# Kernel tuning notes

Measured on AMD Instinct MI355X. Metric: run time of the kernel, lower is better.

The kernel has to match this reference:

```python
import jax, jax.numpy as jnp
import numpy as np

N_NODES = 100000


def _segment_softmax(logits, seg, num_segments):
    # numerically stable softmax of per-edge logits grouped by destination node
    m = jax.ops.segment_max(logits, seg, num_segments=num_segments)
    e = jnp.exp(logits - m[seg])
    s = jax.ops.segment_sum(e, seg, num_segments=num_segments)
    return e / s[seg]


def _cgat(x, W, b, src, dst, edge_attr, num_nodes):
    # get_edge_att: softmax of edge_attr over edges sharing a destination node
    att = _segment_softmax(edge_attr, dst, num_nodes)
    xw = x @ W.T                                  # [N, out]
    msg = att[:, None] * xw[src]                  # gather + scale  [E, out]
    aggr = jax.ops.segment_sum(msg, dst, num_segments=num_nodes)  # scatter-add
    out = aggr + xw + b                           # update(aggr, x) then + bias
    return jax.nn.sigmoid(out)


def setup_inputs() -> dict:
    key = jax.random.key(0)
    k1, k2, k3, k4, k5, k6 = jax.random.split(key, 6)
    in_c, hid_c, out_c = 128, 64, 64
    n_edges = 1600000
    x = jax.random.normal(k1, (N_NODES, in_c), dtype=jnp.float32)
    edge_index = jax.random.randint(k2, (2, n_edges), 0, N_NODES, dtype=jnp.int64)
    edge_attr = jax.random.uniform(k3, (n_edges,), dtype=jnp.float32)
    W1 = jax.random.normal(k4, (hid_c, in_c), dtype=jnp.float32) / np.sqrt(in_c)
    b1 = jnp.zeros((hid_c,), dtype=jnp.float32)
    W2 = jax.random.normal(k5, (out_c, hid_c), dtype=jnp.float32) / np.sqrt(hid_c)
    b2 = jnp.zeros((out_c,), dtype=jnp.float32)
    return {"x": x, "edge_index": edge_index, "edge_attr": edge_attr,
            "W1": W1, "b1": b1, "W2": W2, "b2": b2}


def reference(x, edge_index, edge_attr, W1, b1, W2, b2):
    src, dst = edge_index[0], edge_index[1]
    h1 = _cgat(x, W1, b1, src, dst, edge_attr, N_NODES)
    h2 = _cgat(h1, W2, b2, src, dst, edge_attr, N_NODES)
    return h2
```

## Files before the change

### kernel.cpp

```cpp
#include <hip/hip_runtime.h>
#include <hip/hip_bf16.h>

#define N_NODES 100000
#define N_EDGES 1600000
#define IN_C 128
#define C 64
#define NBKT 196
#define CAP 9216
#define BCHK 6400
#define NBB (N_EDGES / BCHK)
#define GB1 (N_NODES / 32)

typedef float vfloat2 __attribute__((ext_vector_type(2)));

__device__ __forceinline__ float bfu2f(unsigned short u) {
    return __uint_as_float(((unsigned int)u) << 16);
}
__device__ __forceinline__ unsigned short f2bfu(float f) {
    __hip_bfloat16 h = __float2bfloat16(f);
    unsigned short u; __builtin_memcpy(&u, &h, 2); return u;
}
__device__ __forceinline__ float blo(unsigned int v) { return __uint_as_float(v << 16); }
__device__ __forceinline__ float bhi(unsigned int v) { return __uint_as_float(v & 0xFFFF0000u); }
__device__ __forceinline__ float dec_w(unsigned int p) {
    return __uint_as_float(((p & 0x7FFFu) + 0x1FC000u) << 9);
}
__device__ __forceinline__ float load_f(const void* p, int i, int f32) {
    return f32 ? ((const float*)p)[i] : bfu2f(((const unsigned short*)p)[i]);
}
__device__ __forceinline__ int load_idx(const void* ei, size_t i, int i64) {
    return i64 ? (int)((const long long*)ei)[i] : ((const int*)ei)[i];
}

__global__ __launch_bounds__(256) void k_detect(
    const uint4* __restrict__ x4, const int* __restrict__ ei32,
    int* __restrict__ flags)
{
    __shared__ int cff, cnz;
    int t = threadIdx.x;
    if (t == 0) { cff = 0; cnz = 0; }
    __syncthreads();
    int lff = 0;
    #pragma unroll
    for (int j = 0; j < 16; ++j) {
        uint4 w = x4[t + j * 256];
        unsigned int a[4] = {w.x, w.y, w.z, w.w};
        #pragma unroll
        for (int q = 0; q < 4; ++q) {
            if ((a[q] & 0x00007F80u) == 0x00007F80u) lff++;
            if ((a[q] & 0x7F800000u) == 0x7F800000u) lff++;
        }
    }
    int lnz = 0;
    for (int i = t; i < 2048; i += 256)
        if (ei32[2 * i + 1] != 0) lnz++;
    if (lff) atomicAdd(&cff, lff);
    if (lnz) atomicAdd(&cnz, lnz);
    __syncthreads();
    if (t == 0) {
        flags[0] = (cff > 0) ? 1 : 0;
        flags[1] = (cnz == 0) ? 1 : 0;
    }
}

#define W1_STRIDE (IN_C + 4)
__global__ __launch_bounds__(256) void k_build_gemm1(
    const void* __restrict__ ea, const void* __restrict__ ei,
    const int* __restrict__ flags, int* __restrict__ gcnt,
    int2* __restrict__ bkt,
    const void* __restrict__ x, const void* __restrict__ W,
    unsigned short* __restrict__ xw)
{
    __shared__ __align__(16) char smem[56576];
    int t = threadIdx.x;
    if (blockIdx.x < NBB) {
        int2* stage = (int2*)smem;
        int*  h     = (int*)(smem + 51200);
        int*  ex    = (int*)(smem + 52224);
        int*  gb    = (int*)(smem + 53248);
        int*  ps    = (int*)(smem + 54272);
        int*  rk    = (int*)(smem + 55296);
        h[t] = 0; rk[t] = 0;
        __syncthreads();
        int i64 = flags[1], f32 = flags[0];
        int base = blockIdx.x * BCHK;
        for (int i = 0; i < 25; ++i) {
            int e = base + i * 256 + t;
            int d = load_idx(ei, (size_t)N_EDGES + e, i64);
            atomicAdd(&h[d >> 9], 1);
        }
        __syncthreads();
        int hv = h[t];
        ps[t] = hv;
        for (int off = 1; off < 256; off <<= 1) {
            __syncthreads();
            int val = (t >= off) ? ps[t - off] : 0;
            __syncthreads();
            ps[t] += val;
        }
        __syncthreads();
        ex[t] = ps[t] - hv;
        if (t < NBKT) gb[t] = atomicAdd(&gcnt[t], hv);
        __syncthreads();
        for (int i = 0; i < 25; ++i) {
            int e = base + i * 256 + t;
            int d = load_idx(ei, (size_t)N_EDGES + e, i64);
            int s = load_idx(ei, (size_t)e, i64);
            float w = expf(load_f(ea, e, f32));
            unsigned int wb = __float_as_uint(w);
            int wq = (int)((wb + 0x100u) >> 9) - 0x1FC000;
            wq = wq < 0 ? 0 : (wq > 0x7FFF ? 0x7FFF : wq);
            int bk2 = d >> 9;
            int r = atomicAdd(&rk[bk2], 1);
            stage[ex[bk2] + r] =
                make_int2((int)(((unsigned int)s << 15) | (unsigned int)wq), d);
        }
        __syncthreads();
        for (int i = 0; i < 25; ++i) {
            int idx = i * 256 + t;
            int2 r = stage[idx];
            int bk2 = ((unsigned int)r.y) >> 9;
            int lr = idx - ex[bk2];
            int gi = gb[bk2] + lr;
            if (gi < CAP)
                bkt[(size_t)bk2 * CAP + gi] = r;
        }
    } else {
        int bx = blockIdx.x - NBB;
        float* Wls = (float*)smem;
        float* xs  = (float*)(smem + 33792);
        int f32 = flags[0];
        size_t xbase = (size_t)bx * 32 * IN_C;
        if (f32) {
            const float* xp = (const float*)x + xbase;
            #pragma unroll
            for (int j = 0; j < 16; ++j) { int i = t + j * 256; xs[i] = xp[i]; }
            const float* wp = (const float*)W;
            #pragma unroll
            for (int j = 0; j < 32; ++j) {
                int i = t + j * 256;
                Wls[(i >> 7) * W1_STRIDE + (i & 127)] = wp[i];
            }
        } else {
            const unsigned int* xp = (const unsigned int*)((const unsigned short*)x + xbase);
            #pragma unroll
            for (int j = 0; j < 8; ++j) {
                int i = t + j * 256;
                unsigned int v = xp[i];
                xs[2 * i]     = blo(v);
                xs[2 * i + 1] = bhi(v);
            }
            const unsigned short* wp = (const unsigned short*)W;
            #pragma unroll
            for (int j = 0; j < 32; ++j) {
                int i = t + j * 256;
                Wls[(i >> 7) * W1_STRIDE + (i & 127)] = bfu2f(wp[i]);
            }
        }
        __syncthreads();
        int col = t & 63, wv = t >> 6;
        const float* wr = Wls + col * W1_STRIDE;
        const float* xr = xs + wv * 8 * IN_C;
        float acc[8];
        #pragma unroll
        for (int n = 0; n < 8; ++n) acc[n] = 0.f;
        #pragma unroll
        for (int kk = 0; kk < IN_C / 4; ++kk) {
            float4 w4 = *(const float4*)(wr + kk * 4);
            #pragma unroll
            for (int n = 0; n < 8; ++n) {
                float4 x4 = *(const float4*)(xr + n * IN_C + kk * 4);
                acc[n] += x4.x * w4.x + x4.y * w4.y + x4.z * w4.z + x4.w * w4.w;
            }
        }
        size_t obase = (size_t)bx * 32 * C + wv * 8 * C + col;
        #pragma unroll
        for (int n = 0; n < 8; ++n) xw[obase + n * C] = f2bfu(acc[n]);
    }
}

__global__ __launch_bounds__(256) void k_fine(
    const int2* __restrict__ bkt, const int* __restrict__ gcnt,
    int* __restrict__ row_ptr, unsigned int* __restrict__ srt)
{
    __shared__ int h[512], ex[512], ps[256];
    __shared__ int sh_cb;
    int t = threadIdx.x, b = blockIdx.x;
    int v = (t < NBKT) ? gcnt[t] : 0;
    ps[t] = v;
    for (int off = 1; off < 256; off <<= 1) {
        __syncthreads();
        int val = (t >= off) ? ps[t - off] : 0;
        __syncthreads();
        ps[t] += val;
    }
    __syncthreads();
    if (t == b) sh_cb = ps[t] - v;
    if (b == 0 && t == 0) row_ptr[N_NODES] = N_EDGES;
    h[t] = 0; h[t + 256] = 0;
    __syncthreads();
    int nrec = gcnt[b];
    nrec = nrec < CAP ? nrec : CAP;
    int cb = sh_cb;
    const int2* bp = bkt + (size_t)b * CAP;
    for (int i = t; i < nrec; i += 256)
        atomicAdd(&h[bp[i].y & 511], 1);
    __syncthreads();
    int s0 = h[2 * t], s1 = h[2 * t + 1];
    ps[t] = s0 + s1;
    for (int off = 1; off < 256; off <<= 1) {
        __syncthreads();
        int val = (t >= off) ? ps[t - off] : 0;
        __syncthreads();
        ps[t] += val;
    }
    __syncthreads();
    int pe = t ? ps[t - 1] : 0;
    ex[2 * t] = pe; ex[2 * t + 1] = pe + s0;
    __syncthreads();
    int d0 = b * 512 + t;
    if (d0 < N_NODES) row_ptr[d0] = cb + ex[t];
    int d1 = d0 + 256;
    if (d1 < N_NODES) row_ptr[d1] = cb + ex[t + 256];
    h[t] = 0; h[t + 256] = 0;
    __syncthreads();
    for (int i = t; i < nrec; i += 256) {
        int2 r = bp[i];
        int dl = r.y & 511;
        int rk = atomicAdd(&h[dl], 1);
        srt[cb + ex[dl] + rk] = (unsigned int)r.x;
    }
}

#define W2_STRIDE (C + 4)
__global__ __launch_bounds__(256) void k_gemm2(
    const unsigned int* __restrict__ h, const void* __restrict__ W,
    const int* __restrict__ flags, unsigned short* __restrict__ xw)
{
    __shared__ float Wls[C * W2_STRIDE];
    __shared__ float xs[32 * C];
    int t = threadIdx.x;
    size_t dwbase = (size_t)blockIdx.x * 32 * 32;
    #pragma unroll
    for (int j = 0; j < 4; ++j) {
        int i = t + j * 256;
        unsigned int v = h[dwbase + i];
        xs[2 * i]     = blo(v);
        xs[2 * i + 1] = bhi(v);
    }
    if (flags[0]) {
        const float* wp = (const float*)W;
        #pragma unroll
        for (int j = 0; j < 16; ++j) {
            int i = t + j * 256;
            Wls[(i >> 6) * W2_STRIDE + (i & 63)] = wp[i];
        }
    } else {
        const unsigned short* wp = (const unsigned short*)W;
        #pragma unroll
        for (int j = 0; j < 16; ++j) {
            int i = t + j * 256;
            Wls[(i >> 6) * W2_STRIDE + (i & 63)] = bfu2f(wp[i]);
        }
    }
    __syncthreads();
    int col = t & 63, wv = t >> 6;
    const float* wr = Wls + col * W2_STRIDE;
    const float* xr = xs + wv * 8 * C;
    float acc[8];
    #pragma unroll
    for (int n = 0; n < 8; ++n) acc[n] = 0.f;
    #pragma unroll
    for (int kk = 0; kk < C / 4; ++kk) {
        float4 w4 = *(const float4*)(wr + kk * 4);
        #pragma unroll
        for (int n = 0; n < 8; ++n) {
            float4 x4 = *(const float4*)(xr + n * C + kk * 4);
            acc[n] += x4.x * w4.x + x4.y * w4.y + x4.z * w4.z + x4.w * w4.w;
        }
    }
    size_t obase = (size_t)blockIdx.x * 32 * C + wv * 8 * C + col;
    #pragma unroll
    for (int n = 0; n < 8; ++n) xw[obase + n * C] = f2bfu(acc[n]);
}

__global__ __launch_bounds__(256) void k_msg_csr(
    const unsigned int* __restrict__ xw, const unsigned int* __restrict__ srt,
    const int* __restrict__ row_ptr, const void* __restrict__ b,
    const int* __restrict__ flags, void* __restrict__ outp, int out_is_final)
{
    int d = blockIdx.x * 4 + (threadIdx.x >> 6);
    int lane = threadIdx.x & 63;
    int half = lane >> 5, li = lane & 31;
    int beg = row_ptr[d], end = row_ptr[d + 1];
    float accx = 0.f, accy = 0.f, asum = 0.f;
    int j = beg;
    for (; j + 8 <= end; j += 8) {
        int jb = j + 4 * half;
        unsigned int p0 = __builtin_nontemporal_load(srt + jb);
        unsigned int p1 = __builtin_nontemporal_load(srt + jb + 1);
        unsigned int p2 = __builtin_nontemporal_load(srt + jb + 2);
        unsigned int p3 = __builtin_nontemporal_load(srt + jb + 3);
        unsigned int v0 = xw[(size_t)(p0 >> 15) * 32 + li];
        unsigned int v1 = xw[(size_t)(p1 >> 15) * 32 + li];
        unsigned int v2 = xw[(size_t)(p2 >> 15) * 32 + li];
        unsigned int v3 = xw[(size_t)(p3 >> 15) * 32 + li];
        float w0 = dec_w(p0), w1 = dec_w(p1), w2 = dec_w(p2), w3 = dec_w(p3);
        accx += w0 * blo(v0) + w1 * blo(v1) + w2 * blo(v2) + w3 * blo(v3);
        accy += w0 * bhi(v0) + w1 * bhi(v1) + w2 * bhi(v2) + w3 * bhi(v3);
        asum += (w0 + w1) + (w2 + w3);
    }
    if (j + 4 <= end) {
        int jb = j + 2 * half;
        unsigned int p0 = __builtin_nontemporal_load(srt + jb);
        unsigned int p1 = __builtin_nontemporal_load(srt + jb + 1);
        unsigned int v0 = xw[(size_t)(p0 >> 15) * 32 + li];
        unsigned int v1 = xw[(size_t)(p1 >> 15) * 32 + li];
        float w0 = dec_w(p0), w1 = dec_w(p1);
        accx += w0 * blo(v0) + w1 * blo(v1);
        accy += w0 * bhi(v0) + w1 * bhi(v1);
        asum += w0 + w1;
        j += 4;
    }
    if (j + 2 <= end) {
        unsigned int p0 = __builtin_nontemporal_load(srt + j + half);
        unsigned int v0 = xw[(size_t)(p0 >> 15) * 32 + li];
        float w0 = dec_w(p0);
        accx += w0 * blo(v0);
        accy += w0 * bhi(v0);
        asum += w0;
        j += 2;
    }
    if (j < end && half == 0) {
        unsigned int p0 = __builtin_nontemporal_load(srt + j);
        unsigned int v0 = xw[(size_t)(p0 >> 15) * 32 + li];
        float w0 = dec_w(p0);
        accx += w0 * blo(v0);
        accy += w0 * bhi(v0);
        asum += w0;
    }
    accx += __shfl_xor(accx, 32);
    accy += __shfl_xor(accy, 32);
    asum += __shfl_xor(asum, 32);
    float inv = (end > beg) ? 1.f / asum : 0.f;
    unsigned int sv = xw[(size_t)d * 32 + li];
    int f32 = flags[0];
    float b0 = load_f(b, 2 * li, f32), b1 = load_f(b, 2 * li + 1, f32);
    float v0 = accx * inv + blo(sv) + b0;
    float v1 = accy * inv + bhi(sv) + b1;
    float r0 = 1.f / (1.f + expf(-v0));
    float r1 = 1.f / (1.f + expf(-v1));
    if (half == 0) {
        if (out_is_final && f32) {
            vfloat2 rv; rv.x = r0; rv.y = r1;
            __builtin_nontemporal_store(rv, (vfloat2*)outp + (size_t)d * 32 + li);
        } else {
            unsigned int packed = (unsigned int)f2bfu(r0) | ((unsigned int)f2bfu(r1) << 16);
            __builtin_nontemporal_store(packed, (unsigned int*)outp + (size_t)d * 32 + li);
        }
    }
}

extern "C" void kernel_launch(void* const* d_in, const int* in_sizes, int n_in,
                              void* d_out, int out_size, void* d_ws, size_t ws_size,
                              hipStream_t stream) {
    const void* x  = d_in[0];
    const void* ei = d_in[1];
    const void* ea = d_in[2];
    const void* W1 = d_in[3];
    const void* b1 = d_in[4];
    const void* W2 = d_in[5];
    const void* b2 = d_in[6];

    char* base = (char*)d_ws;
    int*            flags   = (int*)base;
    int*            gcnt    = (int*)(base + 256);
    int*            row_ptr = (int*)(base + 4096);
    unsigned int*   srt     = (unsigned int*)(base + 405504);
    int2*           bkt     = (int2*)(base + 6805504);
    unsigned short* h1      = (unsigned short*)(base + 6805504);
    unsigned short* xw      = (unsigned short*)(base + 21256192);

    k_detect<<<1, 256, 0, stream>>>((const uint4*)x, (const int*)ei, flags);
    hipMemsetAsync(gcnt, 0, 1024, stream);

    k_build_gemm1<<<NBB + GB1, 256, 0, stream>>>(ea, ei, flags, gcnt, bkt,
                                                 x, W1, xw);
    k_fine<<<NBKT, 256, 0, stream>>>(bkt, gcnt, row_ptr, srt);

    k_msg_csr<<<N_NODES / 4, 256, 0, stream>>>((const unsigned int*)xw, srt, row_ptr, b1, flags, h1, 0);

    k_gemm2<<<N_NODES / 32, 256, 0, stream>>>((const unsigned int*)h1, W2, flags, xw);
    k_msg_csr<<<N_NODES / 4, 256, 0, stream>>>((const unsigned int*)xw, srt, row_ptr, b2, flags, d_out, 1);
}
```

Baseline: 324.7 us.

## Shrink build/gemm1 shared memory for occupancy and fold gcnt zeroing into detect

Reduces the bucketing chunk from 6400 to 4000 edges per block and splits the GEMM1 weight staging into two 32-column halves, cutting static shared memory from about 56KB to about 37KB so more blocks can be resident per CU. The zeroing of the global bucket counters moves from a separate memset into the detect kernel, removing one launch. The GEMM now loads W twice with extra barriers and each thread computes fewer outputs, which lowers reuse per block.

```diff
diff --git a/kernel.cpp b/kernel.cpp
--- a/kernel.cpp
+++ b/kernel.cpp
@@ -7,7 +7,7 @@
 #define C 64
 #define NBKT 196
 #define CAP 9216
-#define BCHK 6400
+#define BCHK 4000
 #define NBB (N_EDGES / BCHK)
 #define GB1 (N_NODES / 32)
 
@@ -34,10 +34,11 @@
 
 __global__ __launch_bounds__(256) void k_detect(
     const uint4* __restrict__ x4, const int* __restrict__ ei32,
-    int* __restrict__ flags)
+    int* __restrict__ flags, int* __restrict__ gcnt)
 {
     __shared__ int cff, cnz;
     int t = threadIdx.x;
+    gcnt[t] = 0;
     if (t == 0) { cff = 0; cnz = 0; }
     __syncthreads();
     int lff = 0;
@@ -71,23 +72,26 @@
     const void* __restrict__ x, const void* __restrict__ W,
     unsigned short* __restrict__ xw)
 {
-    __shared__ __align__(16) char smem[56576];
+    __shared__ __align__(16) char smem[37120];
     int t = threadIdx.x;
     if (blockIdx.x < NBB) {
         int2* stage = (int2*)smem;
-        int*  h     = (int*)(smem + 51200);
-        int*  ex    = (int*)(smem + 52224);
-        int*  gb    = (int*)(smem + 53248);
-        int*  ps    = (int*)(smem + 54272);
-        int*  rk    = (int*)(smem + 55296);
+        int*  h     = (int*)(smem + 32000);
+        int*  ex    = (int*)(smem + 33024);
+        int*  gb    = (int*)(smem + 34048);
+        int*  ps    = (int*)(smem + 35072);
+        int*  rk    = (int*)(smem + 36096);
         h[t] = 0; rk[t] = 0;
         __syncthreads();
         int i64 = flags[1], f32 = flags[0];
         int base = blockIdx.x * BCHK;
-        for (int i = 0; i < 25; ++i) {
-            int e = base + i * 256 + t;
-            int d = load_idx(ei, (size_t)N_EDGES + e, i64);
-            atomicAdd(&h[d >> 9], 1);
+        #pragma unroll
+        for (int i = 0; i < 16; ++i) {
+            int ii = i * 256 + t;
+            if (ii < BCHK) {
+                int d = load_idx(ei, (size_t)N_EDGES + base + ii, i64);
+                atomicAdd(&h[d >> 9], 1);
+            }
         }
         __syncthreads();
         int hv = h[t];
@@ -102,45 +106,46 @@
         ex[t] = ps[t] - hv;
         if (t < NBKT) gb[t] = atomicAdd(&gcnt[t], hv);
         __syncthreads();
-        for (int i = 0; i < 25; ++i) {
-            int e = base + i * 256 + t;
-            int d = load_idx(ei, (size_t)N_EDGES + e, i64);
-            int s = load_idx(ei, (size_t)e, i64);
-            float w = expf(load_f(ea, e, f32));
-            unsigned int wb = __float_as_uint(w);
-            int wq = (int)((wb + 0x100u) >> 9) - 0x1FC000;
-            wq = wq < 0 ? 0 : (wq > 0x7FFF ? 0x7FFF : wq);
-            int bk2 = d >> 9;
-            int r = atomicAdd(&rk[bk2], 1);
-            stage[ex[bk2] + r] =
-                make_int2((int)(((unsigned int)s << 15) | (unsigned int)wq), d);
-        }
-        __syncthreads();
-        for (int i = 0; i < 25; ++i) {
+        #pragma unroll
+        for (int i = 0; i < 16; ++i) {
+            int ii = i * 256 + t;
+            if (ii < BCHK) {
+                int e = base + ii;
+                int d = load_idx(ei, (size_t)N_EDGES + e, i64);
+                int s = load_idx(ei, (size_t)e, i64);
+                float w = expf(load_f(ea, e, f32));
+                unsigned int wb = __float_as_uint(w);
+                int wq = (int)((wb + 0x100u) >> 9) - 0x1FC000;
+                wq = wq < 0 ? 0 : (wq > 0x7FFF ? 0x7FFF : wq);
+                int bk2 = d >> 9;
+                int r = atomicAdd(&rk[bk2], 1);
+                stage[ex[bk2] + r] =
+                    make_int2((int)(((unsigned int)s << 15) | (unsigned int)wq), d);
+            }
+        }
+        __syncthreads();
+        #pragma unroll
+        for (int i = 0; i < 16; ++i) {
             int idx = i * 256 + t;
-            int2 r = stage[idx];
-            int bk2 = ((unsigned int)r.y) >> 9;
-            int lr = idx - ex[bk2];
-            int gi = gb[bk2] + lr;
-            if (gi < CAP)
-                bkt[(size_t)bk2 * CAP + gi] = r;
+            if (idx < BCHK) {
+                int2 r = stage[idx];
+                int bk2 = ((unsigned int)r.y) >> 9;
+                int lr = idx - ex[bk2];
+                int gi = gb[bk2] + lr;
+                if (gi < CAP)
+                    bkt[(size_t)bk2 * CAP + gi] = r;
+            }
         }
     } else {
         int bx = blockIdx.x - NBB;
-        float* Wls = (float*)smem;
-        float* xs  = (float*)(smem + 33792);
+        float* xs  = (float*)smem;
+        float* Wls = (float*)(smem + 16384);
         int f32 = flags[0];
         size_t xbase = (size_t)bx * 32 * IN_C;
         if (f32) {
             const float* xp = (const float*)x + xbase;
             #pragma unroll
             for (int j = 0; j < 16; ++j) { int i = t + j * 256; xs[i] = xp[i]; }
-            const float* wp = (const float*)W;
-            #pragma unroll
-            for (int j = 0; j < 32; ++j) {
-                int i = t + j * 256;
-                Wls[(i >> 7) * W1_STRIDE + (i & 127)] = wp[i];
-            }
         } else {
             const unsigned int* xp = (const unsigned int*)((const unsigned short*)x + xbase);
             #pragma unroll
@@ -150,32 +155,45 @@
                 xs[2 * i]     = blo(v);
                 xs[2 * i + 1] = bhi(v);
             }
-            const unsigned short* wp = (const unsigned short*)W;
+        }
+        int col = t & 31, wv = t >> 5;
+        #pragma unroll
+        for (int hf = 0; hf < 2; ++hf) {
+            __syncthreads();
+            if (f32) {
+                const float* wp = (const float*)W + hf * 32 * IN_C;
+                #pragma unroll
+                for (int j = 0; j < 16; ++j) {
+                    int i = t + j * 256;
+                    Wls[(i >> 7) * W1_STRIDE + (i & 127)] = wp[i];
+                }
+            } else {
+                const unsigned short* wp = (const unsigned short*)W + hf * 32 * IN_C;
+                #pragma unroll
+                for (int j = 0; j < 16; ++j) {
+                    int i = t + j * 256;
+                    Wls[(i >> 7) * W1_STRIDE + (i & 127)] = bfu2f(wp[i]);
+                }
+            }
+            __syncthreads();
+            const float* wr = Wls + col * W1_STRIDE;
+            const float* xr = xs + wv * 4 * IN_C;
+            float acc[4];
             #pragma unroll
-            for (int j = 0; j < 32; ++j) {
-                int i = t + j * 256;
-                Wls[(i >> 7) * W1_STRIDE + (i & 127)] = bfu2f(wp[i]);
-            }
-        }
-        __syncthreads();
-        int col = t & 63, wv = t >> 6;
-        const float* wr = Wls + col * W1_STRIDE;
-        const float* xr = xs + wv * 8 * IN_C;
-        float acc[8];
-        #pragma unroll
-        for (int n = 0; n < 8; ++n) acc[n] = 0.f;
-        #pragma unroll
-        for (int kk = 0; kk < IN_C / 4; ++kk) {
-            float4 w4 = *(const float4*)(wr + kk * 4);
+            for (int n = 0; n < 4; ++n) acc[n] = 0.f;
             #pragma unroll
-            for (int n = 0; n < 8; ++n) {
-                float4 x4 = *(const float4*)(xr + n * IN_C + kk * 4);
-                acc[n] += x4.x * w4.x + x4.y * w4.y + x4.z * w4.z + x4.w * w4.w;
-            }
-        }
-        size_t obase = (size_t)bx * 32 * C + wv * 8 * C + col;
-        #pragma unroll
-        for (int n = 0; n < 8; ++n) xw[obase + n * C] = f2bfu(acc[n]);
+            for (int kk = 0; kk < IN_C / 4; ++kk) {
+                float4 w4 = *(const float4*)(wr + kk * 4);
+                #pragma unroll
+                for (int n = 0; n < 4; ++n) {
+                    float4 x4 = *(const float4*)(xr + n * IN_C + kk * 4);
+                    acc[n] += x4.x * w4.x + x4.y * w4.y + x4.z * w4.z + x4.w * w4.w;
+                }
+            }
+            size_t obase = (size_t)bx * 32 * C + wv * 4 * C + hf * 32 + col;
+            #pragma unroll
+            for (int n = 0; n < 4; ++n) xw[obase + n * C] = f2bfu(acc[n]);
+        }
     }
 }
 
@@ -381,8 +399,7 @@
     unsigned short* h1      = (unsigned short*)(base + 6805504);
     unsigned short* xw      = (unsigned short*)(base + 21256192);
 
-    k_detect<<<1, 256, 0, stream>>>((const uint4*)x, (const int*)ei, flags);
-    hipMemsetAsync(gcnt, 0, 1024, stream);
+    k_detect<<<1, 256, 0, stream>>>((const uint4*)x, (const int*)ei, flags, gcnt);
 
     k_build_gemm1<<<NBB + GB1, 256, 0, stream>>>(ea, ei, flags, gcnt, bkt,
                                                  x, W1, xw);
```

Result: faster. 316.0 us (-2.7%).
